# Kernel optimization log

Hardware: AMD Instinct MI355X
Metric: run time of the kernel (lower is better)

The kernel has to match this reference:

```python
import jax, jax.numpy as jnp
import numpy as np

B = 4096

def _conv(x, w, s):
    return jax.lax.conv_general_dilated(x, w, (s, s), 'SAME', dimension_numbers=('NHWC', 'HWIO', 'NHWC'))

def _convT(x, w, s):
    return jax.lax.conv_transpose(x, w, (s, s), 'SAME', dimension_numbers=('NHWC', 'HWIO', 'NHWC'))

def _otsu(error):
    # faithful to the TF source: 81 candidate thresholds in [0.1, 0.9],
    # counts of NONZERO masked entries (not simple class counts), NaN-guarded means,
    thresholds = jnp.asarray(np.arange(0.1, 0.91, 0.01), dtype=jnp.float32)  # 81
    hw = error.shape[1] * error.shape[2]
    zero = jnp.zeros(error.shape[0], jnp.float32)

    def step(carry, t):
        sig_max, opti = carry
        below = error < t
        e0 = jnp.where(below, error, 0.0)
        e1 = jnp.where(below, 0.0, error)
        n0 = jnp.sum((e0 != 0).astype(jnp.float32), axis=(1, 2))
        n1 = jnp.sum((e1 != 0).astype(jnp.float32), axis=(1, 2))
        m0 = (jnp.sum(e0, axis=(1, 2)) / hw) * ((n1 + n0) / n0)
        m0 = jnp.where(jnp.isnan(m0), 0.0, m0)
        m1 = (jnp.sum(e1, axis=(1, 2)) / hw) * ((n1 + n0) / n1)
        m1 = jnp.where(jnp.isnan(m1), 0.0, m1)
        p0 = n0 / (n0 + n1)
        p1 = n1 / (n0 + n1)
        sig_b = p0 * p1 * (m0 - m1) ** 2
        upd = sig_b >= sig_max
        return (jnp.where(upd, sig_b, sig_max), jnp.where(upd, t, opti)), None

    (_, opti), _ = jax.lax.scan(step, (zero, zero), thresholds)
    return opti

def _forward(x, eps_noise, ew1, eb1, es1, eo1, ew2, eb2, es2, eo2, ew3, eb3, es3, eo3,
             wzm, bzm, wzl, bzl, dw, db, tw1, tb1, ds1, do1, tw2, tb2, ds2, do2,
             tw3, tb3, ds3, do3, tw4, tb4):
    relu = jax.nn.relu
    # encoder; inference-mode BatchNorm folded into per-channel scale/offset
    h = relu(_conv(x, ew1, 2) + eb1) * es1 + eo1            # [B,16,16,32]
    h = relu(_conv(h, ew2, 2) + eb2) * es2 + eo2            # [B,8,8,64]
    h = relu(_conv(h, ew3, 2) + eb3) * es3 + eo3            # [B,4,4,128]
    h = h.reshape(h.shape[0], -1)                           # [B,2048]
    z_mean = relu(h @ wzm + bzm)
    z_log_var = relu(h @ wzl + bzl)
    z = z_mean + jnp.exp(0.5 * z_log_var) * eps_noise       # Sampling layer
    # decoder (Dropout is identity at inference)
    d = relu(z @ dw + db).reshape(-1, 8, 8, 128)
    d = relu(_convT(d, tw1, 1) + tb1) * ds1 + do1           # [B,8,8,128]
    d = relu(_convT(d, tw2, 2) + tb2) * ds2 + do2           # [B,16,16,64]
    d = relu(_convT(d, tw3, 2) + tb3) * ds3 + do3           # [B,32,32,32]
    recon = jax.nn.sigmoid(_convT(d, tw4, 1) + tb4)         # [B,32,32,3]
    error = jnp.mean((x - recon) ** 2, axis=-1)             # [B,32,32]
    thresh = _otsu(error)                                   # [B]
    return error < thresh[:, None, None]                    # bool mask

def setup_inputs():
    key = jax.random.key(0)
    ks = jax.random.split(key, 12)
    f = jnp.float32
    s = 0.05  # small init scale to keep activations sane
    d = {}
    d['x'] = jax.random.uniform(ks[0], (B, 32, 32, 3), f)
    d['eps_noise'] = jax.random.normal(ks[1], (B, 128), f)
    d['ew1'] = jax.random.normal(ks[2], (5, 5, 3, 32), f) * s
    d['eb1'] = jnp.zeros((32,), f); d['es1'] = jnp.ones((32,), f); d['eo1'] = jnp.zeros((32,), f)
    d['ew2'] = jax.random.normal(ks[3], (5, 5, 32, 64), f) * s
    d['eb2'] = jnp.zeros((64,), f); d['es2'] = jnp.ones((64,), f); d['eo2'] = jnp.zeros((64,), f)
    d['ew3'] = jax.random.normal(ks[4], (5, 5, 64, 128), f) * s
    d['eb3'] = jnp.zeros((128,), f); d['es3'] = jnp.ones((128,), f); d['eo3'] = jnp.zeros((128,), f)
    d['wzm'] = jax.random.normal(ks[5], (2048, 128), f) * s
    d['bzm'] = jnp.zeros((128,), f)
    d['wzl'] = jax.random.normal(ks[6], (2048, 128), f) * s
    d['bzl'] = jnp.zeros((128,), f)
    d['dw'] = jax.random.normal(ks[7], (128, 8192), f) * s
    d['db'] = jnp.zeros((8192,), f)
    d['tw1'] = jax.random.normal(ks[8], (1, 1, 128, 128), f) * s
    d['tb1'] = jnp.zeros((128,), f); d['ds1'] = jnp.ones((128,), f); d['do1'] = jnp.zeros((128,), f)
    d['tw2'] = jax.random.normal(ks[9], (3, 3, 128, 64), f) * s
    d['tb2'] = jnp.zeros((64,), f); d['ds2'] = jnp.ones((64,), f); d['do2'] = jnp.zeros((64,), f)
    d['tw3'] = jax.random.normal(ks[10], (3, 3, 64, 32), f) * s
    d['tb3'] = jnp.zeros((32,), f); d['ds3'] = jnp.ones((32,), f); d['do3'] = jnp.zeros((32,), f)
    d['tw4'] = jax.random.normal(ks[11], (3, 3, 32, 3), f) * s
    d['tb4'] = jnp.zeros((3,), f)
    return d

def reference(x, eps_noise, ew1, eb1, es1, eo1, ew2, eb2, es2, eo2, ew3, eb3, es3, eo3,
              wzm, bzm, wzl, bzl, dw, db, tw1, tb1, ds1, do1, tw2, tb2, ds2, do2,
              tw3, tb3, ds3, do3, tw4, tb4):
    mask = _forward(x, eps_noise, ew1, eb1, es1, eo1, ew2, eb2, es2, eo2, ew3, eb3, es3, eo3,
                    wzm, bzm, wzl, bzl, dw, db, tw1, tb1, ds1, do1, tw2, tb2, ds2, do2,
                    tw3, tb3, ds3, do3, tw4, tb4)
    return mask.astype(jnp.int32)
```

## Files before the change

### kernel.cpp

```cpp
#include <hip/hip_runtime.h>
#include <cstdint>
#include <cstddef>


__global__ __launch_bounds__(256) void k_conv1(const float* __restrict__ x,
    const float* __restrict__ w, const float* __restrict__ bb,
    const float* __restrict__ sc, const float* __restrict__ of,
    float* __restrict__ out) {
  const int b = blockIdx.x;
  const int pos = threadIdx.x;
  const int oy = pos >> 4, ox = pos & 15;
  float acc[32];
#pragma unroll
  for (int c = 0; c < 32; ++c) acc[c] = 0.f;
  const float* xb = x + (size_t)b * 3072;
#pragma unroll 1
  for (int ky = 0; ky < 5; ++ky) {
    const int iy = 2 * oy - 1 + ky;
    if ((unsigned)iy >= 32u) continue;
#pragma unroll 1
    for (int kx = 0; kx < 5; ++kx) {
      const int ix = 2 * ox - 1 + kx;
      if ((unsigned)ix >= 32u) continue;
      const float* xp = xb + (iy * 32 + ix) * 3;
#pragma unroll
      for (int ci = 0; ci < 3; ++ci) {
        const float v = xp[ci];
        const float* wp = w + ((ky * 5 + kx) * 3 + ci) * 32;
#pragma unroll
        for (int c = 0; c < 32; ++c) acc[c] = fmaf(v, wp[c], acc[c]);
      }
    }
  }
  float* op = out + ((size_t)b * 256 + pos) * 32;
#pragma unroll
  for (int c = 0; c < 32; ++c) {
    const float v = fmaxf(acc[c] + bb[c], 0.f);
    op[c] = v * sc[c] + of[c];
  }
}

__global__ __launch_bounds__(256) void k_conv2(const float* __restrict__ in,
    const float* __restrict__ w, const float* __restrict__ bb,
    const float* __restrict__ sc, const float* __restrict__ of,
    float* __restrict__ out) {
  __shared__ float4 tile4[2048];
  const int b = blockIdx.x;
  const int tid = threadIdx.x;
#pragma unroll
  for (int q = 0; q < 8; ++q) {
    const int f4 = tid + q * 256;
    const int pix = f4 >> 3, g4 = f4 & 7;
    const int s4 = (((pix >> 4) * 5) + (pix & 15)) & 7;
    tile4[pix * 8 + (g4 ^ s4)] = ((const float4*)(in + (size_t)b * 8192))[f4];
  }
  __syncthreads();
  const int pos = tid & 63;
  const int chg = __builtin_amdgcn_readfirstlane(tid >> 6);
  const int co0 = chg * 16;
  const int oy = pos >> 3, ox = pos & 7;
  float acc[16];
#pragma unroll
  for (int c = 0; c < 16; ++c) acc[c] = 0.f;
#pragma unroll 1
  for (int ky = 0; ky < 5; ++ky) {
    const int iy = 2 * oy - 1 + ky;
#pragma unroll 1
    for (int kx = 0; kx < 5; ++kx) {
      const int ix = 2 * ox - 1 + kx;
      const bool valid = ((unsigned)iy < 16u) && ((unsigned)ix < 16u);
      const int pix = valid ? (iy * 16 + ix) : 0;
      const int s4 = (((pix >> 4) * 5) + (pix & 15)) & 7;
      const float* wt = w + ((size_t)(ky * 5 + kx) * 32) * 64 + co0;
#pragma unroll
      for (int g4 = 0; g4 < 8; ++g4) {
        float4 a = tile4[pix * 8 + (g4 ^ s4)];
        a.x = valid ? a.x : 0.f; a.y = valid ? a.y : 0.f;
        a.z = valid ? a.z : 0.f; a.w = valid ? a.w : 0.f;
        const float av[4] = {a.x, a.y, a.z, a.w};
#pragma unroll
        for (int j = 0; j < 4; ++j) {
          const float* wp = wt + (g4 * 4 + j) * 64;
#pragma unroll
          for (int c = 0; c < 16; ++c) acc[c] = fmaf(av[j], wp[c], acc[c]);
        }
      }
    }
  }
  float* op = out + ((size_t)b * 64 + pos) * 64 + co0;
#pragma unroll
  for (int c = 0; c < 16; ++c) {
    const float v = fmaxf(acc[c] + bb[co0 + c], 0.f);
    op[c] = v * sc[co0 + c] + of[co0 + c];
  }
}

__global__ __launch_bounds__(512) void k_conv3(const float* __restrict__ in,
    const float* __restrict__ w, const float* __restrict__ bb,
    const float* __restrict__ sc, const float* __restrict__ of,
    float* __restrict__ out) {
  __shared__ float4 tile4[4096];
  const int b0 = blockIdx.x * 4;
  const int tid = threadIdx.x;
#pragma unroll
  for (int q = 0; q < 8; ++q) {
    const int f4 = tid + q * 512;
    const int img = f4 >> 10, rem = f4 & 1023;
    const int pix = rem >> 4, g4 = rem & 15;
    const int s4 = (((pix >> 3) * 5) + (pix & 7) + img * 3) & 15;
    tile4[img * 1024 + pix * 16 + (g4 ^ s4)] =
        ((const float4*)(in + (size_t)(b0 + img) * 4096))[rem];
  }
  __syncthreads();
  const int lane = tid & 63;
  const int img = lane >> 4, pos = lane & 15;
  const int chg = __builtin_amdgcn_readfirstlane(tid >> 6);
  const int co0 = chg * 16;
  const int oy = pos >> 2, ox = pos & 3;
  float acc[16];
#pragma unroll
  for (int c = 0; c < 16; ++c) acc[c] = 0.f;
  const float4* tb = &tile4[img * 1024];
#pragma unroll 1
  for (int ky = 0; ky < 5; ++ky) {
    const int iy = 2 * oy - 1 + ky;
#pragma unroll 1
    for (int kx = 0; kx < 5; ++kx) {
      const int ix = 2 * ox - 1 + kx;
      const bool valid = ((unsigned)iy < 8u) && ((unsigned)ix < 8u);
      const int pix = valid ? (iy * 8 + ix) : 0;
      const int s4 = (((pix >> 3) * 5) + (pix & 7) + img * 3) & 15;
      const float* wt = w + ((size_t)(ky * 5 + kx) * 64) * 128 + co0;
#pragma unroll
      for (int g4 = 0; g4 < 16; ++g4) {
        float4 a = tb[pix * 16 + (g4 ^ s4)];
        a.x = valid ? a.x : 0.f; a.y = valid ? a.y : 0.f;
        a.z = valid ? a.z : 0.f; a.w = valid ? a.w : 0.f;
        const float av[4] = {a.x, a.y, a.z, a.w};
#pragma unroll
        for (int j = 0; j < 4; ++j) {
          const float* wp = wt + (g4 * 4 + j) * 128;
#pragma unroll
          for (int c = 0; c < 16; ++c) acc[c] = fmaf(av[j], wp[c], acc[c]);
        }
      }
    }
  }
  float* op = out + ((size_t)(b0 + img) * 16 + pos) * 128 + co0;
#pragma unroll
  for (int c = 0; c < 16; ++c) {
    const float v = fmaxf(acc[c] + bb[co0 + c], 0.f);
    op[c] = v * sc[co0 + c] + of[co0 + c];
  }
}

__global__ __launch_bounds__(256) void k_fcz(const float* __restrict__ h3,
    const float* __restrict__ wzm, const float* __restrict__ bzm,
    const float* __restrict__ wzl, const float* __restrict__ bzl,
    const float* __restrict__ eps, float* __restrict__ z) {
  __shared__ float a[4 * 256];
  const int ib = blockIdx.x * 4;
  const int tid = threadIdx.x;
  const int co = tid & 127;
  const int grp = __builtin_amdgcn_readfirstlane(tid >> 7);
  float am[2], al[2];
#pragma unroll
  for (int i = 0; i < 2; ++i) { am[i] = 0.f; al[i] = 0.f; }
  for (int kc = 0; kc < 2048; kc += 256) {
    __syncthreads();
    {
      const int r = tid >> 6, c4 = (tid & 63) << 2;
      *(float4*)&a[r * 256 + c4] =
          *(const float4*)&h3[(size_t)(ib + r) * 2048 + kc + c4];
    }
    __syncthreads();
#pragma unroll 4
    for (int k = 0; k < 256; k += 4) {
      float wm[4], wl[4];
#pragma unroll
      for (int q = 0; q < 4; ++q) {
        wm[q] = wzm[(size_t)(kc + k + q) * 128 + co];
        wl[q] = wzl[(size_t)(kc + k + q) * 128 + co];
      }
#pragma unroll
      for (int i = 0; i < 2; ++i) {
        const float4 av = *(const float4*)&a[(grp * 2 + i) * 256 + k];
        am[i] = fmaf(av.x, wm[0], am[i]); am[i] = fmaf(av.y, wm[1], am[i]);
        am[i] = fmaf(av.z, wm[2], am[i]); am[i] = fmaf(av.w, wm[3], am[i]);
        al[i] = fmaf(av.x, wl[0], al[i]); al[i] = fmaf(av.y, wl[1], al[i]);
        al[i] = fmaf(av.z, wl[2], al[i]); al[i] = fmaf(av.w, wl[3], al[i]);
      }
    }
  }
#pragma unroll
  for (int i = 0; i < 2; ++i) {
    const int row = ib + grp * 2 + i;
    const float zm = fmaxf(am[i] + bzm[co], 0.f);
    const float zl = fmaxf(al[i] + bzl[co], 0.f);
    z[(size_t)row * 128 + co] = zm + expf(0.5f * zl) * eps[(size_t)row * 128 + co];
  }
}

__global__ __launch_bounds__(256) void k_fcdec(const float* __restrict__ z,
    const float* __restrict__ dw, const float* __restrict__ db,
    float* __restrict__ out) {
  __shared__ float4 zt4[2048];
  const int bid = blockIdx.x;
  const int m0 = (bid >> 6) * 64;
  const int n0 = (bid & 63) * 128;
  const int tid = threadIdx.x;
#pragma unroll
  for (int q = 0; q < 8; ++q) {
    const int f4 = tid + q * 256;
    const int img = f4 >> 5, g4 = f4 & 31;
    const int s4 = (img * 5) & 31;
    zt4[img * 32 + (g4 ^ s4)] = ((const float4*)(z + (size_t)(m0) * 128))[f4];
  }
  __syncthreads();
  const int img = tid & 63;
  const int grp = __builtin_amdgcn_readfirstlane(tid >> 6);
  const int nb = n0 + grp * 32;
  const int s4 = (img * 5) & 31;
  float acc[32];
#pragma unroll
  for (int c = 0; c < 32; ++c) acc[c] = 0.f;
#pragma unroll
  for (int g4 = 0; g4 < 32; ++g4) {
    const float4 a = zt4[img * 32 + (g4 ^ s4)];
    const float av[4] = {a.x, a.y, a.z, a.w};
#pragma unroll
    for (int j = 0; j < 4; ++j) {
      const float* wp = dw + (size_t)(g4 * 4 + j) * 8192 + nb;
#pragma unroll
      for (int c = 0; c < 32; ++c) acc[c] = fmaf(av[j], wp[c], acc[c]);
    }
  }
  float* op = out + (size_t)(m0 + img) * 8192 + nb;
#pragma unroll
  for (int c = 0; c < 32; ++c) op[c] = fmaxf(acc[c] + db[nb + c], 0.f);
}

__global__ __launch_bounds__(256) void k_tconv1(const float* __restrict__ in,
    const float* __restrict__ w, const float* __restrict__ bb,
    const float* __restrict__ sc, const float* __restrict__ of,
    float* __restrict__ out) {
  __shared__ float4 tile4[2048];
  const int b = blockIdx.x;
  const int tid = threadIdx.x;
#pragma unroll
  for (int q = 0; q < 8; ++q) {
    const int f4 = tid + q * 256;
    const int pix = f4 >> 5, g4 = f4 & 31;
    const int s4 = (pix * 5) & 31;
    tile4[pix * 32 + (g4 ^ s4)] = ((const float4*)(in + (size_t)b * 8192))[f4];
  }
  __syncthreads();
  const int pos = tid & 63;
  const int chg = __builtin_amdgcn_readfirstlane(tid >> 6);
  const int co0 = chg * 32;
  const int s4 = (pos * 5) & 31;
  float acc[32];
#pragma unroll
  for (int c = 0; c < 32; ++c) acc[c] = 0.f;
#pragma unroll
  for (int g4 = 0; g4 < 32; ++g4) {
    const float4 a = tile4[pos * 32 + (g4 ^ s4)];
    const float av[4] = {a.x, a.y, a.z, a.w};
#pragma unroll
    for (int j = 0; j < 4; ++j) {
      const float* wp = w + (g4 * 4 + j) * 128 + co0;
#pragma unroll
      for (int c = 0; c < 32; ++c) acc[c] = fmaf(av[j], wp[c], acc[c]);
    }
  }
  float* op = out + ((size_t)b * 64 + pos) * 128 + co0;
#pragma unroll
  for (int c = 0; c < 32; ++c) {
    const float v = fmaxf(acc[c] + bb[co0 + c], 0.f);
    op[c] = v * sc[co0 + c] + of[co0 + c];
  }
}

__global__ __launch_bounds__(256) void k_tconv2(const float* __restrict__ in,
    const float* __restrict__ w, const float* __restrict__ bb,
    const float* __restrict__ sc, const float* __restrict__ of,
    float* __restrict__ t2g) {
  __shared__ float4 tile4[2048];
  const int b = blockIdx.x;
  const int tid = threadIdx.x;
#pragma unroll
  for (int q = 0; q < 8; ++q) {
    const int f4 = tid + q * 256;
    const int pix = f4 >> 5, g4 = f4 & 31;
    const int s4 = (pix * 5) & 31;
    tile4[pix * 32 + (g4 ^ s4)] = ((const float4*)(in + (size_t)b * 8192))[f4];
  }
  __syncthreads();
  const int pos = tid & 63;
  const int chg = __builtin_amdgcn_readfirstlane(tid >> 6);
  const int co0 = chg * 16;
  const int jy = pos >> 3, jx = pos & 7;
  float acc[4][16];
#pragma unroll
  for (int p = 0; p < 4; ++p)
#pragma unroll
    for (int c = 0; c < 16; ++c) acc[p][c] = 0.f;
  const int DY[9]  = {1,1,0,0,1,0,0,0,0};
  const int DX[9]  = {1,0,1,0,0,0,1,0,0};
  const int KYt[9] = {0,0,2,2,0,2,1,1,1};
  const int KXt[9] = {0,2,0,2,1,1,0,2,1};
  const int PHt[9] = {0,0,0,0,1,1,2,2,3};
#pragma unroll
  for (int t = 0; t < 9; ++t) {
    const int sy = jy - DY[t], sx = jx - DX[t];
    const bool valid = (sy >= 0) && (sx >= 0);
    const int pix = valid ? (sy * 8 + sx) : 0;
    const int s4 = (pix * 5) & 31;
    const int ph = PHt[t];
    const float* wt = w + ((size_t)(KYt[t] * 3 + KXt[t]) * 128) * 64 + co0;
#pragma unroll 2
    for (int g4 = 0; g4 < 32; ++g4) {
      float4 a = tile4[pix * 32 + (g4 ^ s4)];
      a.x = valid ? a.x : 0.f; a.y = valid ? a.y : 0.f;
      a.z = valid ? a.z : 0.f; a.w = valid ? a.w : 0.f;
      const float av[4] = {a.x, a.y, a.z, a.w};
#pragma unroll
      for (int j = 0; j < 4; ++j) {
        const float* wp = wt + (g4 * 4 + j) * 64;
#pragma unroll
        for (int c = 0; c < 16; ++c) acc[ph][c] = fmaf(av[j], wp[c], acc[ph][c]);
      }
    }
  }
#pragma unroll
  for (int py = 0; py < 2; ++py) {
    const int oy = 2 * jy + py;
    float vv[32];
#pragma unroll
    for (int px = 0; px < 2; ++px)
#pragma unroll
      for (int c = 0; c < 16; ++c) {
        const float v = fmaxf(acc[py * 2 + px][c] + bb[co0 + c], 0.f);
        vv[px * 16 + c] = v * sc[co0 + c] + of[co0 + c];
      }
    float* op = t2g + (((size_t)b * 4 + chg) * 256 + oy * 16 + 2 * jx) * 16;
#pragma unroll
    for (int q = 0; q < 8; ++q)
      *(float4*)&op[q * 4] = make_float4(vv[q*4+0], vv[q*4+1], vv[q*4+2], vv[q*4+3]);
  }
}

__global__ __launch_bounds__(512) void k_tconv3(const float* __restrict__ t2g,
    const float* __restrict__ w, const float* __restrict__ bb,
    const float* __restrict__ sc, const float* __restrict__ of,
    float* __restrict__ t3g) {
  __shared__ float4 tile4[145 * 16];
  const int b = blockIdx.x >> 1;
  const int r0 = (blockIdx.x & 1) * 8;
  const int tid = threadIdx.x;
  for (int f4 = tid; f4 < 2304; f4 += 512) {
    const int rr = f4 >> 8;
    const int col = (f4 >> 4) & 15, g4 = f4 & 15;
    const int gy = r0 - 1 + rr;
    float4 v = make_float4(0.f, 0.f, 0.f, 0.f);
    if (gy >= 0)
      v = ((const float4*)t2g)[(((size_t)b * 4 + (g4 >> 2)) * 256
                                + gy * 16 + col) * 4 + (g4 & 3)];
    const int s4 = (rr * 5 + col) & 15;
    tile4[(rr * 16 + col) * 16 + (g4 ^ s4)] = v;
  }
  if (tid < 16) tile4[144 * 16 + tid] = make_float4(0.f, 0.f, 0.f, 0.f);
  __syncthreads();
  const int pos = tid & 127;
  const int prow = pos >> 4, pcol = pos & 15;
  const int chg = __builtin_amdgcn_readfirstlane(tid >> 7);
  const int co0 = chg * 8;
  float acc[4][8];
#pragma unroll
  for (int p = 0; p < 4; ++p)
#pragma unroll
    for (int c = 0; c < 8; ++c) acc[p][c] = 0.f;
  const int DY[9]  = {1,1,0,0,1,0,0,0,0};
  const int DX[9]  = {1,0,1,0,0,0,1,0,0};
  const int KYt[9] = {0,0,2,2,0,2,1,1,1};
  const int KXt[9] = {0,2,0,2,1,1,0,2,1};
  const int PHt[9] = {0,0,0,0,1,1,2,2,3};
#pragma unroll
  for (int t = 0; t < 9; ++t) {
    const int syst = prow + 1 - DY[t];
    const int sx = pcol - DX[t];
    const bool vx = (sx >= 0);
    const int pix = vx ? (syst * 16 + sx) : 144;
    const int s4 = vx ? ((syst * 5 + sx) & 15) : 0;
    const int ph = PHt[t];
    const float* wt = w + ((size_t)(KYt[t] * 3 + KXt[t]) * 64) * 32 + co0;
#pragma unroll 2
    for (int g4 = 0; g4 < 16; ++g4) {
      const float4 a = tile4[pix * 16 + (g4 ^ s4)];
      const float av[4] = {a.x, a.y, a.z, a.w};
#pragma unroll
      for (int j = 0; j < 4; ++j) {
        const float* wp = wt + (g4 * 4 + j) * 32;
#pragma unroll
        for (int c = 0; c < 8; ++c) acc[ph][c] = fmaf(av[j], wp[c], acc[ph][c]);
      }
    }
  }
  const int jy = r0 + prow;
#pragma unroll
  for (int py = 0; py < 2; ++py)
#pragma unroll
    for (int px = 0; px < 2; ++px) {
      const int oy = 2 * jy + py, ox = 2 * pcol + px;
      float* op = t3g + ((size_t)b * 4 + chg) * 8192 + (size_t)(oy * 32 + ox) * 8;
      float vv[8];
#pragma unroll
      for (int c = 0; c < 8; ++c) {
        const float v = fmaxf(acc[py * 2 + px][c] + bb[co0 + c], 0.f);
        vv[c] = v * sc[co0 + c] + of[co0 + c];
      }
      *(float4*)&op[0] = make_float4(vv[0], vv[1], vv[2], vv[3]);
      *(float4*)&op[4] = make_float4(vv[4], vv[5], vv[6], vv[7]);
    }
}

__global__ __launch_bounds__(256) void k_tconv4err(const float* __restrict__ t3g,
    const float* __restrict__ w, const float* __restrict__ bb,
    const float* __restrict__ x, float* __restrict__ err) {
  __shared__ float4 win4[34 * 65];
  const int b = blockIdx.x;
  const int tid = threadIdx.x;
  const int ty = tid >> 4, tx = tid & 15;
  float acc[2][2][3];
#pragma unroll
  for (int dy = 0; dy < 2; ++dy)
#pragma unroll
    for (int dx = 0; dx < 2; ++dx)
#pragma unroll
      for (int c = 0; c < 3; ++c) acc[dy][dx][c] = 0.f;
#pragma unroll 1
  for (int g = 0; g < 4; ++g) {
    __syncthreads();
    for (int f4 = tid; f4 < 2176; f4 += 256) {
      const int rr = f4 >> 6;
      const int rem = f4 & 63;
      const int col = rem >> 1, h = rem & 1;
      const int gy = rr - 1;
      float4 v = make_float4(0.f, 0.f, 0.f, 0.f);
      if ((unsigned)gy < 32u)
        v = ((const float4*)(t3g + ((size_t)b * 4 + g) * 8192))[(gy * 32 + col) * 2 + h];
      win4[rr * 65 + col * 2 + h] = v;
    }
    __syncthreads();
#pragma unroll 1
    for (int h = 0; h < 2; ++h) {
      float4 W[4][4];
#pragma unroll
      for (int wy = 0; wy < 4; ++wy)
#pragma unroll
        for (int wx = 0; wx < 4; ++wx) {
          const int col = 2 * tx - 1 + wx;
          const bool edge = (wx == 0) || (wx == 3);
          const bool v = edge ? ((unsigned)col < 32u) : true;
          const int cc = v ? col : 0;
          float4 t = win4[(2 * ty + wy) * 65 + cc * 2 + h];
          if (edge) {
            t.x = v ? t.x : 0.f; t.y = v ? t.y : 0.f;
            t.z = v ? t.z : 0.f; t.w = v ? t.w : 0.f;
          }
          W[wy][wx] = t;
        }
#pragma unroll
      for (int j = 0; j < 4; ++j) {
        const int ci = g * 8 + h * 4 + j;
#pragma unroll
        for (int ky = 0; ky < 3; ++ky)
#pragma unroll
          for (int kx = 0; kx < 3; ++kx) {
            const float* wp = w + ((ky * 3 + kx) * 32 + ci) * 3;
            const float w0 = wp[0], w1 = wp[1], w2 = wp[2];
#pragma unroll
            for (int dy = 0; dy < 2; ++dy)
#pragma unroll
              for (int dx = 0; dx < 2; ++dx) {
                const float4 t = W[dy + ky][dx + kx];
                const float av = (j == 0) ? t.x : (j == 1) ? t.y : (j == 2) ? t.z : t.w;
                acc[dy][dx][0] = fmaf(av, w0, acc[dy][dx][0]);
                acc[dy][dx][1] = fmaf(av, w1, acc[dy][dx][1]);
                acc[dy][dx][2] = fmaf(av, w2, acc[dy][dx][2]);
              }
          }
      }
    }
  }
#pragma unroll
  for (int dy = 0; dy < 2; ++dy)
#pragma unroll
    for (int dx = 0; dx < 2; ++dx) {
      const int oy = 2 * ty + dy, ox = 2 * tx + dx;
      const size_t pidx = (size_t)b * 1024 + oy * 32 + ox;
      float e = 0.f;
#pragma unroll
      for (int c = 0; c < 3; ++c) {
        const float pre = acc[dy][dx][c] + bb[c];
        float r;
        if (pre >= 0.f) {
          r = 1.f / (1.f + expf(-pre));
        } else {
          const float ex = expf(pre);
          r = ex / (1.f + ex);
        }
        const float dd = x[pidx * 3 + c] - r;
        e += dd * dd;
      }
      err[pidx] = e / 3.0f;
    }
}

__global__ __launch_bounds__(256) void k_otsu(const float* __restrict__ err,
                                              int* __restrict__ outmask) {
  __shared__ float e[2][1024];
  __shared__ float sig[2][81];
  __shared__ float opti[2];
  const int b0 = blockIdx.x * 2;
  const int tid = threadIdx.x;
  for (int f4 = tid; f4 < 512; f4 += 256) {
    const int img = f4 >> 8, idx = (f4 & 255) << 2;
    *(float4*)&e[img][idx] = *(const float4*)&err[(size_t)(b0 + img) * 1024 + idx];
  }
  __syncthreads();
  const int img = tid >> 7, j = tid & 127;
  if (j < 81) {
    const float t = (float)(0.1 + (double)j * 0.01);
    float n0 = 0.f, n1 = 0.f, s0 = 0.f, s1 = 0.f;
    for (int i = 0; i < 1024; ++i) {
      const float v = e[img][i];
      if (v < t) {
        if (v != 0.f) { n0 += 1.f; s0 += v; }
      } else {
        n1 += 1.f; s1 += v;
      }
    }
    const float nt = n0 + n1;
    float m0 = (s0 / 1024.f) * (nt / n0);
    if (m0 != m0) m0 = 0.f;
    float m1 = (s1 / 1024.f) * (nt / n1);
    if (m1 != m1) m1 = 0.f;
    const float p0 = n0 / nt, p1 = n1 / nt;
    const float dm = m0 - m1;
    sig[img][j] = p0 * p1 * (dm * dm);
  }
  __syncthreads();
  if (j == 0) {
    float smax = 0.f, op = 0.f;
    for (int jj = 0; jj < 81; ++jj) {
      const float sb = sig[img][jj];
      const float t = (float)(0.1 + (double)jj * 0.01);
      if (sb >= smax) { smax = sb; op = t; }
    }
    opti[img] = op;
  }
  __syncthreads();
#pragma unroll
  for (int q = 0; q < 8; ++q) {
    const int idx = tid + q * 256;
    const int im = idx >> 10, p = idx & 1023;
    outmask[(size_t)(b0 + im) * 1024 + p] = (e[im][p] < opti[im]) ? 1 : 0;
  }
}

extern "C" void kernel_launch(void* const* d_in, const int* in_sizes, int n_in,
                              void* d_out, int out_size, void* d_ws, size_t ws_size,
                              hipStream_t stream) {
  (void)in_sizes; (void)n_in; (void)out_size;
  const float* x    = (const float*)d_in[0];
  const float* eps  = (const float*)d_in[1];
  const float* ew1  = (const float*)d_in[2];
  const float* eb1  = (const float*)d_in[3];
  const float* es1  = (const float*)d_in[4];
  const float* eo1  = (const float*)d_in[5];
  const float* ew2  = (const float*)d_in[6];
  const float* eb2  = (const float*)d_in[7];
  const float* es2  = (const float*)d_in[8];
  const float* eo2  = (const float*)d_in[9];
  const float* ew3  = (const float*)d_in[10];
  const float* eb3  = (const float*)d_in[11];
  const float* es3  = (const float*)d_in[12];
  const float* eo3  = (const float*)d_in[13];
  const float* wzm  = (const float*)d_in[14];
  const float* bzm  = (const float*)d_in[15];
  const float* wzl  = (const float*)d_in[16];
  const float* bzl  = (const float*)d_in[17];
  const float* dw   = (const float*)d_in[18];
  const float* db   = (const float*)d_in[19];
  const float* tw1  = (const float*)d_in[20];
  const float* tb1  = (const float*)d_in[21];
  const float* ds1  = (const float*)d_in[22];
  const float* do1  = (const float*)d_in[23];
  const float* tw2  = (const float*)d_in[24];
  const float* tb2  = (const float*)d_in[25];
  const float* ds2  = (const float*)d_in[26];
  const float* do2  = (const float*)d_in[27];
  const float* tw3  = (const float*)d_in[28];
  const float* tb3  = (const float*)d_in[29];
  const float* ds3  = (const float*)d_in[30];
  const float* do3  = (const float*)d_in[31];
  const float* tw4  = (const float*)d_in[32];
  const float* tb4  = (const float*)d_in[33];
  int* mask = (int*)d_out;

  const size_t per_img_bytes = 233472;
  int C = 64;
  const int cand[6] = {4096, 2048, 1024, 512, 256, 128};
  for (int i = 0; i < 6; ++i) {
    if ((size_t)cand[i] * per_img_bytes <= ws_size) { C = cand[i]; break; }
  }

  float* p0 = (float*)d_ws;
  float* p1 = p0 + (size_t)C * 32768;
  float* p2 = p1 + (size_t)C * 8192;
  float* p3 = p2 + (size_t)C * 16384;

  for (int c0 = 0; c0 < 4096; c0 += C) {
    const float* xc   = x   + (size_t)c0 * 3072;
    const float* epsc = eps + (size_t)c0 * 128;
    int*         mc   = mask + (size_t)c0 * 1024;
    float* h1 = p0;  float* dd = p0;  float* t3 = p0;
    float* h2 = p1;  float* zz = p1;  float* t1 = p1;
    float* h3 = p2;  float* t2 = p2;
    float* er = p3;

    k_conv1    <<<C,      256, 0, stream>>>(xc, ew1, eb1, es1, eo1, h1);
    k_conv2    <<<C,      256, 0, stream>>>(h1, ew2, eb2, es2, eo2, h2);
    k_conv3    <<<C / 4,  512, 0, stream>>>(h2, ew3, eb3, es3, eo3, h3);
    k_fcz      <<<C / 4,  256, 0, stream>>>(h3, wzm, bzm, wzl, bzl, epsc, zz);
    k_fcdec    <<<C,      256, 0, stream>>>(zz, dw, db, dd);
    k_tconv1   <<<C,      256, 0, stream>>>(dd, tw1, tb1, ds1, do1, t1);
    k_tconv2   <<<C,      256, 0, stream>>>(t1, tw2, tb2, ds2, do2, t2);
    k_tconv3   <<<C * 2,  512, 0, stream>>>(t2, tw3, tb3, ds3, do3, t3);
    k_tconv4err<<<C,      256, 0, stream>>>(t3, tw4, tb4, xc, er);
    k_otsu     <<<C / 2,  256, 0, stream>>>(er, mc);
  }
}
```

Before: 3.809 ms.

## Split conv and tconv kernels across output-channel halves and shrink workspace via ping-pong

Each conv/tconv kernel now launches twice as many blocks, with each block computing half of the output channels (and tconv4err computing half the rows). Fewer accumulators per thread mean more parallelism and lower register pressure. Intermediate activations use channel-group-blocked layouts written with float4 stores, and the workspace is reduced to two ping-pong buffers so larger chunks fit. The cost is that each input tile is loaded into shared memory twice, once per half.

```diff
diff --git a/kernel.cpp b/kernel.cpp
--- a/kernel.cpp
+++ b/kernel.cpp
@@ -43,9 +43,10 @@
 __global__ __launch_bounds__(256) void k_conv2(const float* __restrict__ in,
     const float* __restrict__ w, const float* __restrict__ bb,
     const float* __restrict__ sc, const float* __restrict__ of,
-    float* __restrict__ out) {
+    float* __restrict__ h2g) {
   __shared__ float4 tile4[2048];
-  const int b = blockIdx.x;
+  const int b = blockIdx.x >> 1;
+  const int cobase = (blockIdx.x & 1) * 32;
   const int tid = threadIdx.x;
 #pragma unroll
   for (int q = 0; q < 8; ++q) {
@@ -57,11 +58,11 @@
   __syncthreads();
   const int pos = tid & 63;
   const int chg = __builtin_amdgcn_readfirstlane(tid >> 6);
-  const int co0 = chg * 16;
+  const int co0 = cobase + chg * 8;
   const int oy = pos >> 3, ox = pos & 7;
-  float acc[16];
-#pragma unroll
-  for (int c = 0; c < 16; ++c) acc[c] = 0.f;
+  float acc[8];
+#pragma unroll
+  for (int c = 0; c < 8; ++c) acc[c] = 0.f;
 #pragma unroll 1
   for (int ky = 0; ky < 5; ++ky) {
     const int iy = 2 * oy - 1 + ky;
@@ -82,25 +83,29 @@
         for (int j = 0; j < 4; ++j) {
           const float* wp = wt + (g4 * 4 + j) * 64;
 #pragma unroll
-          for (int c = 0; c < 16; ++c) acc[c] = fmaf(av[j], wp[c], acc[c]);
+          for (int c = 0; c < 8; ++c) acc[c] = fmaf(av[j], wp[c], acc[c]);
         }
       }
     }
   }
-  float* op = out + ((size_t)b * 64 + pos) * 64 + co0;
-#pragma unroll
-  for (int c = 0; c < 16; ++c) {
+  float vv[8];
+#pragma unroll
+  for (int c = 0; c < 8; ++c) {
     const float v = fmaxf(acc[c] + bb[co0 + c], 0.f);
-    op[c] = v * sc[co0 + c] + of[co0 + c];
-  }
-}
-
-__global__ __launch_bounds__(512) void k_conv3(const float* __restrict__ in,
+    vv[c] = v * sc[co0 + c] + of[co0 + c];
+  }
+  float* op = h2g + (((size_t)b * 8 + (co0 >> 3)) * 64 + pos) * 8;
+  *(float4*)&op[0] = make_float4(vv[0], vv[1], vv[2], vv[3]);
+  *(float4*)&op[4] = make_float4(vv[4], vv[5], vv[6], vv[7]);
+}
+
+__global__ __launch_bounds__(512) void k_conv3(const float* __restrict__ h2g,
     const float* __restrict__ w, const float* __restrict__ bb,
     const float* __restrict__ sc, const float* __restrict__ of,
     float* __restrict__ out) {
   __shared__ float4 tile4[4096];
-  const int b0 = blockIdx.x * 4;
+  const int b0 = (blockIdx.x >> 1) * 4;
+  const int cobase = (blockIdx.x & 1) * 64;
   const int tid = threadIdx.x;
 #pragma unroll
   for (int q = 0; q < 8; ++q) {
@@ -109,17 +114,18 @@
     const int pix = rem >> 4, g4 = rem & 15;
     const int s4 = (((pix >> 3) * 5) + (pix & 7) + img * 3) & 15;
     tile4[img * 1024 + pix * 16 + (g4 ^ s4)] =
-        ((const float4*)(in + (size_t)(b0 + img) * 4096))[rem];
+        ((const float4*)h2g)[((size_t)(b0 + img) * 8 + (g4 >> 1)) * 128
+                             + pix * 2 + (g4 & 1)];
   }
   __syncthreads();
   const int lane = tid & 63;
   const int img = lane >> 4, pos = lane & 15;
   const int chg = __builtin_amdgcn_readfirstlane(tid >> 6);
-  const int co0 = chg * 16;
+  const int co0 = cobase + chg * 8;
   const int oy = pos >> 2, ox = pos & 3;
-  float acc[16];
-#pragma unroll
-  for (int c = 0; c < 16; ++c) acc[c] = 0.f;
+  float acc[8];
+#pragma unroll
+  for (int c = 0; c < 8; ++c) acc[c] = 0.f;
   const float4* tb = &tile4[img * 1024];
 #pragma unroll 1
   for (int ky = 0; ky < 5; ++ky) {
@@ -141,17 +147,20 @@
         for (int j = 0; j < 4; ++j) {
           const float* wp = wt + (g4 * 4 + j) * 128;
 #pragma unroll
-          for (int c = 0; c < 16; ++c) acc[c] = fmaf(av[j], wp[c], acc[c]);
+          for (int c = 0; c < 8; ++c) acc[c] = fmaf(av[j], wp[c], acc[c]);
         }
       }
     }
   }
   float* op = out + ((size_t)(b0 + img) * 16 + pos) * 128 + co0;
-#pragma unroll
-  for (int c = 0; c < 16; ++c) {
+  float vv[8];
+#pragma unroll
+  for (int c = 0; c < 8; ++c) {
     const float v = fmaxf(acc[c] + bb[co0 + c], 0.f);
-    op[c] = v * sc[co0 + c] + of[co0 + c];
-  }
+    vv[c] = v * sc[co0 + c] + of[co0 + c];
+  }
+  *(float4*)&op[0] = make_float4(vv[0], vv[1], vv[2], vv[3]);
+  *(float4*)&op[4] = make_float4(vv[4], vv[5], vv[6], vv[7]);
 }
 
 __global__ __launch_bounds__(256) void k_fcz(const float* __restrict__ h3,
@@ -243,9 +252,10 @@
 __global__ __launch_bounds__(256) void k_tconv1(const float* __restrict__ in,
     const float* __restrict__ w, const float* __restrict__ bb,
     const float* __restrict__ sc, const float* __restrict__ of,
-    float* __restrict__ out) {
+    float* __restrict__ t1g) {
   __shared__ float4 tile4[2048];
-  const int b = blockIdx.x;
+  const int b = blockIdx.x >> 1;
+  const int cobase = (blockIdx.x & 1) * 64;
   const int tid = threadIdx.x;
 #pragma unroll
   for (int q = 0; q < 8; ++q) {
@@ -257,11 +267,11 @@
   __syncthreads();
   const int pos = tid & 63;
   const int chg = __builtin_amdgcn_readfirstlane(tid >> 6);
-  const int co0 = chg * 32;
+  const int co0 = cobase + chg * 16;
   const int s4 = (pos * 5) & 31;
-  float acc[32];
-#pragma unroll
-  for (int c = 0; c < 32; ++c) acc[c] = 0.f;
+  float acc[16];
+#pragma unroll
+  for (int c = 0; c < 16; ++c) acc[c] = 0.f;
 #pragma unroll
   for (int g4 = 0; g4 < 32; ++g4) {
     const float4 a = tile4[pos * 32 + (g4 ^ s4)];
@@ -270,41 +280,48 @@
     for (int j = 0; j < 4; ++j) {
       const float* wp = w + (g4 * 4 + j) * 128 + co0;
 #pragma unroll
-      for (int c = 0; c < 32; ++c) acc[c] = fmaf(av[j], wp[c], acc[c]);
-    }
-  }
-  float* op = out + ((size_t)b * 64 + pos) * 128 + co0;
-#pragma unroll
-  for (int c = 0; c < 32; ++c) {
+      for (int c = 0; c < 16; ++c) acc[c] = fmaf(av[j], wp[c], acc[c]);
+    }
+  }
+  float vv[16];
+#pragma unroll
+  for (int c = 0; c < 16; ++c) {
     const float v = fmaxf(acc[c] + bb[co0 + c], 0.f);
-    op[c] = v * sc[co0 + c] + of[co0 + c];
-  }
-}
-
-__global__ __launch_bounds__(256) void k_tconv2(const float* __restrict__ in,
+    vv[c] = v * sc[co0 + c] + of[co0 + c];
+  }
+  float* op = t1g + (((size_t)b * 8 + (co0 >> 4)) * 64 + pos) * 16;
+#pragma unroll
+  for (int q = 0; q < 4; ++q)
+    *(float4*)&op[q * 4] = make_float4(vv[q*4+0], vv[q*4+1], vv[q*4+2], vv[q*4+3]);
+}
+
+__global__ __launch_bounds__(256) void k_tconv2(const float* __restrict__ t1g,
     const float* __restrict__ w, const float* __restrict__ bb,
     const float* __restrict__ sc, const float* __restrict__ of,
     float* __restrict__ t2g) {
   __shared__ float4 tile4[2048];
-  const int b = blockIdx.x;
+  const int b = blockIdx.x >> 1;
+  const int cobase = (blockIdx.x & 1) * 32;
   const int tid = threadIdx.x;
 #pragma unroll
   for (int q = 0; q < 8; ++q) {
     const int f4 = tid + q * 256;
     const int pix = f4 >> 5, g4 = f4 & 31;
     const int s4 = (pix * 5) & 31;
-    tile4[pix * 32 + (g4 ^ s4)] = ((const float4*)(in + (size_t)b * 8192))[f4];
+    tile4[pix * 32 + (g4 ^ s4)] =
+        ((const float4*)t1g)[((size_t)b * 8 + (g4 >> 2)) * 256
+                             + pix * 4 + (g4 & 3)];
   }
   __syncthreads();
   const int pos = tid & 63;
   const int chg = __builtin_amdgcn_readfirstlane(tid >> 6);
-  const int co0 = chg * 16;
+  const int co0 = cobase + chg * 8;
   const int jy = pos >> 3, jx = pos & 7;
-  float acc[4][16];
+  float acc[4][8];
 #pragma unroll
   for (int p = 0; p < 4; ++p)
 #pragma unroll
-    for (int c = 0; c < 16; ++c) acc[p][c] = 0.f;
+    for (int c = 0; c < 8; ++c) acc[p][c] = 0.f;
   const int DY[9]  = {1,1,0,0,1,0,0,0,0};
   const int DX[9]  = {1,0,1,0,0,0,1,0,0};
   const int KYt[9] = {0,0,2,2,0,2,1,1,1};
@@ -328,24 +345,24 @@
       for (int j = 0; j < 4; ++j) {
         const float* wp = wt + (g4 * 4 + j) * 64;
 #pragma unroll
-        for (int c = 0; c < 16; ++c) acc[ph][c] = fmaf(av[j], wp[c], acc[ph][c]);
+        for (int c = 0; c < 8; ++c) acc[ph][c] = fmaf(av[j], wp[c], acc[ph][c]);
       }
     }
   }
 #pragma unroll
   for (int py = 0; py < 2; ++py) {
     const int oy = 2 * jy + py;
-    float vv[32];
+    float vv[16];
 #pragma unroll
     for (int px = 0; px < 2; ++px)
 #pragma unroll
-      for (int c = 0; c < 16; ++c) {
+      for (int c = 0; c < 8; ++c) {
         const float v = fmaxf(acc[py * 2 + px][c] + bb[co0 + c], 0.f);
-        vv[px * 16 + c] = v * sc[co0 + c] + of[co0 + c];
-      }
-    float* op = t2g + (((size_t)b * 4 + chg) * 256 + oy * 16 + 2 * jx) * 16;
-#pragma unroll
-    for (int q = 0; q < 8; ++q)
+        vv[px * 8 + c] = v * sc[co0 + c] + of[co0 + c];
+      }
+    float* op = t2g + (((size_t)b * 8 + (co0 >> 3)) * 256 + oy * 16 + 2 * jx) * 8;
+#pragma unroll
+    for (int q = 0; q < 4; ++q)
       *(float4*)&op[q * 4] = make_float4(vv[q*4+0], vv[q*4+1], vv[q*4+2], vv[q*4+3]);
   }
 }
@@ -364,8 +381,8 @@
     const int gy = r0 - 1 + rr;
     float4 v = make_float4(0.f, 0.f, 0.f, 0.f);
     if (gy >= 0)
-      v = ((const float4*)t2g)[(((size_t)b * 4 + (g4 >> 2)) * 256
-                                + gy * 16 + col) * 4 + (g4 & 3)];
+      v = ((const float4*)t2g)[(((size_t)b * 8 + (g4 >> 1)) * 256
+                                + gy * 16 + col) * 2 + (g4 & 1)];
     const int s4 = (rr * 5 + col) & 15;
     tile4[(rr * 16 + col) * 16 + (g4 ^ s4)] = v;
   }
@@ -427,25 +444,24 @@
 __global__ __launch_bounds__(256) void k_tconv4err(const float* __restrict__ t3g,
     const float* __restrict__ w, const float* __restrict__ bb,
     const float* __restrict__ x, float* __restrict__ err) {
-  __shared__ float4 win4[34 * 65];
-  const int b = blockIdx.x;
-  const int tid = threadIdx.x;
-  const int ty = tid >> 4, tx = tid & 15;
-  float acc[2][2][3];
+  __shared__ float4 win4[18 * 65];
+  const int b = blockIdx.x >> 1;
+  const int r0 = (blockIdx.x & 1) * 16;
+  const int tid = threadIdx.x;
+  const int tx = tid & 31, ty = tid >> 5;
+  float acc[2][3];
 #pragma unroll
   for (int dy = 0; dy < 2; ++dy)
 #pragma unroll
-    for (int dx = 0; dx < 2; ++dx)
-#pragma unroll
-      for (int c = 0; c < 3; ++c) acc[dy][dx][c] = 0.f;
+    for (int c = 0; c < 3; ++c) acc[dy][c] = 0.f;
 #pragma unroll 1
   for (int g = 0; g < 4; ++g) {
     __syncthreads();
-    for (int f4 = tid; f4 < 2176; f4 += 256) {
+    for (int f4 = tid; f4 < 1152; f4 += 256) {
       const int rr = f4 >> 6;
       const int rem = f4 & 63;
       const int col = rem >> 1, h = rem & 1;
-      const int gy = rr - 1;
+      const int gy = r0 - 1 + rr;
       float4 v = make_float4(0.f, 0.f, 0.f, 0.f);
       if ((unsigned)gy < 32u)
         v = ((const float4*)(t3g + ((size_t)b * 4 + g) * 8192))[(gy * 32 + col) * 2 + h];
@@ -454,67 +470,60 @@
     __syncthreads();
 #pragma unroll 1
     for (int h = 0; h < 2; ++h) {
-      float4 W[4][4];
+      float4 W[4][3];
 #pragma unroll
       for (int wy = 0; wy < 4; ++wy)
 #pragma unroll
-        for (int wx = 0; wx < 4; ++wx) {
-          const int col = 2 * tx - 1 + wx;
-          const bool edge = (wx == 0) || (wx == 3);
-          const bool v = edge ? ((unsigned)col < 32u) : true;
+        for (int wx = 0; wx < 3; ++wx) {
+          const int col = tx - 1 + wx;
+          const bool v = ((unsigned)col < 32u);
           const int cc = v ? col : 0;
           float4 t = win4[(2 * ty + wy) * 65 + cc * 2 + h];
-          if (edge) {
-            t.x = v ? t.x : 0.f; t.y = v ? t.y : 0.f;
-            t.z = v ? t.z : 0.f; t.w = v ? t.w : 0.f;
-          }
+          t.x = v ? t.x : 0.f; t.y = v ? t.y : 0.f;
+          t.z = v ? t.z : 0.f; t.w = v ? t.w : 0.f;
           W[wy][wx] = t;
         }
 #pragma unroll
       for (int j = 0; j < 4; ++j) {
-        const int ci = g * 8 + h * 4 + j;
 #pragma unroll
         for (int ky = 0; ky < 3; ++ky)
 #pragma unroll
           for (int kx = 0; kx < 3; ++kx) {
+            const int ci = g * 8 + h * 4 + j;
             const float* wp = w + ((ky * 3 + kx) * 32 + ci) * 3;
             const float w0 = wp[0], w1 = wp[1], w2 = wp[2];
 #pragma unroll
-            for (int dy = 0; dy < 2; ++dy)
-#pragma unroll
-              for (int dx = 0; dx < 2; ++dx) {
-                const float4 t = W[dy + ky][dx + kx];
-                const float av = (j == 0) ? t.x : (j == 1) ? t.y : (j == 2) ? t.z : t.w;
-                acc[dy][dx][0] = fmaf(av, w0, acc[dy][dx][0]);
-                acc[dy][dx][1] = fmaf(av, w1, acc[dy][dx][1]);
-                acc[dy][dx][2] = fmaf(av, w2, acc[dy][dx][2]);
-              }
+            for (int dy = 0; dy < 2; ++dy) {
+              const float4 t = W[dy + ky][kx];
+              const float av = (j == 0) ? t.x : (j == 1) ? t.y : (j == 2) ? t.z : t.w;
+              acc[dy][0] = fmaf(av, w0, acc[dy][0]);
+              acc[dy][1] = fmaf(av, w1, acc[dy][1]);
+              acc[dy][2] = fmaf(av, w2, acc[dy][2]);
+            }
           }
       }
     }
   }
 #pragma unroll
-  for (int dy = 0; dy < 2; ++dy)
-#pragma unroll
-    for (int dx = 0; dx < 2; ++dx) {
-      const int oy = 2 * ty + dy, ox = 2 * tx + dx;
-      const size_t pidx = (size_t)b * 1024 + oy * 32 + ox;
-      float e = 0.f;
-#pragma unroll
-      for (int c = 0; c < 3; ++c) {
-        const float pre = acc[dy][dx][c] + bb[c];
-        float r;
-        if (pre >= 0.f) {
-          r = 1.f / (1.f + expf(-pre));
-        } else {
-          const float ex = expf(pre);
-          r = ex / (1.f + ex);
-        }
-        const float dd = x[pidx * 3 + c] - r;
-        e += dd * dd;
-      }
-      err[pidx] = e / 3.0f;
-    }
+  for (int dy = 0; dy < 2; ++dy) {
+    const int oy = r0 + 2 * ty + dy;
+    const size_t pidx = (size_t)b * 1024 + oy * 32 + tx;
+    float e = 0.f;
+#pragma unroll
+    for (int c = 0; c < 3; ++c) {
+      const float pre = acc[dy][c] + bb[c];
+      float r;
+      if (pre >= 0.f) {
+        r = 1.f / (1.f + expf(-pre));
+      } else {
+        const float ex = expf(pre);
+        r = ex / (1.f + ex);
+      }
+      const float dd = x[pidx * 3 + c] - r;
+      e += dd * dd;
+    }
+    err[pidx] = e / 3.0f;
+  }
 }
 
 __global__ __launch_bounds__(256) void k_otsu(const float* __restrict__ err,
@@ -609,36 +618,30 @@
   const float* tb4  = (const float*)d_in[33];
   int* mask = (int*)d_out;
 
-  const size_t per_img_bytes = 233472;
+  const size_t per_img_bytes = (16384 + 32768) * 4;
   int C = 64;
   const int cand[6] = {4096, 2048, 1024, 512, 256, 128};
   for (int i = 0; i < 6; ++i) {
     if ((size_t)cand[i] * per_img_bytes <= ws_size) { C = cand[i]; break; }
   }
 
-  float* p0 = (float*)d_ws;
-  float* p1 = p0 + (size_t)C * 32768;
-  float* p2 = p1 + (size_t)C * 8192;
-  float* p3 = p2 + (size_t)C * 16384;
+  float* pA = (float*)d_ws;
+  float* pB = pA + (size_t)C * 16384;
 
   for (int c0 = 0; c0 < 4096; c0 += C) {
     const float* xc   = x   + (size_t)c0 * 3072;
     const float* epsc = eps + (size_t)c0 * 128;
     int*         mc   = mask + (size_t)c0 * 1024;
-    float* h1 = p0;  float* dd = p0;  float* t3 = p0;
-    float* h2 = p1;  float* zz = p1;  float* t1 = p1;
-    float* h3 = p2;  float* t2 = p2;
-    float* er = p3;
-
-    k_conv1    <<<C,      256, 0, stream>>>(xc, ew1, eb1, es1, eo1, h1);
-    k_conv2    <<<C,      256, 0, stream>>>(h1, ew2, eb2, es2, eo2, h2);
-    k_conv3    <<<C / 4,  512, 0, stream>>>(h2, ew3, eb3, es3, eo3, h3);
-    k_fcz      <<<C / 4,  256, 0, stream>>>(h3, wzm, bzm, wzl, bzl, epsc, zz);
-    k_fcdec    <<<C,      256, 0, stream>>>(zz, dw, db, dd);
-    k_tconv1   <<<C,      256, 0, stream>>>(dd, tw1, tb1, ds1, do1, t1);
-    k_tconv2   <<<C,      256, 0, stream>>>(t1, tw2, tb2, ds2, do2, t2);
-    k_tconv3   <<<C * 2,  512, 0, stream>>>(t2, tw3, tb3, ds3, do3, t3);
-    k_tconv4err<<<C,      256, 0, stream>>>(t3, tw4, tb4, xc, er);
-    k_otsu     <<<C / 2,  256, 0, stream>>>(er, mc);
-  }
-}
+
+    k_conv1    <<<C,      256, 0, stream>>>(xc, ew1, eb1, es1, eo1, pA);
+    k_conv2    <<<2 * C,  256, 0, stream>>>(pA, ew2, eb2, es2, eo2, pB);
+    k_conv3    <<<C / 2,  512, 0, stream>>>(pB, ew3, eb3, es3, eo3, pA);
+    k_fcz      <<<C / 4,  256, 0, stream>>>(pA, wzm, bzm, wzl, bzl, epsc, pB);
+    k_fcdec    <<<C,      256, 0, stream>>>(pB, dw, db, pA);
+    k_tconv1   <<<2 * C,  256, 0, stream>>>(pA, tw1, tb1, ds1, do1, pB);
+    k_tconv2   <<<2 * C,  256, 0, stream>>>(pB, tw2, tb2, ds2, do2, pA);
+    k_tconv3   <<<2 * C,  512, 0, stream>>>(pA, tw3, tb3, ds3, do3, pB);
+    k_tconv4err<<<2 * C,  256, 0, stream>>>(pB, tw4, tb4, xc, pA);
+    k_otsu     <<<C / 2,  256, 0, stream>>>(pA, mc);
+  }
+}
```

After: 4.042 ms. 1.06x slower.
